# Kernel tuning notes

Hardware: AMD Instinct MI355X
Metric: run time of the kernel (lower is better)

## Reference

```python
import jax, jax.numpy as jnp
import numpy as np

N, E, DIN, DH, H, B = 50000, 800000, 128, 32, 8, 512
NEG_SLOPE = 0.2


def glorot(key, shape):
    fan_in, fan_out = shape[0], shape[-1]
    lim = (6.0 / (fan_in + fan_out)) ** 0.5
    return jax.random.uniform(key, shape, jnp.float32, -lim, lim)


def setup_inputs() -> dict:
    key = jax.random.key(0)
    ks = jax.random.split(key, 16)
    x = jax.random.normal(ks[0], (N, DIN), jnp.float32)
    edge_index = jax.random.randint(ks[1], (2, E), 0, N, jnp.int64)
    batch = jnp.sort(jax.random.randint(ks[2], (N,), 0, B, jnp.int64))
    edge_weight = jax.random.uniform(ks[3], (E, 1), jnp.float32)
    # layer 1: GATv2Conv(DIN -> DH, heads=H, edge_dim=1)
    Wl1 = glorot(ks[4], (DIN, H * DH))
    Wr1 = glorot(ks[5], (DIN, H * DH))
    We1 = glorot(ks[6], (1, H * DH))
    att1 = glorot(ks[7], (H, DH))
    b1 = jnp.zeros((H * DH,), jnp.float32)
    # layer 2: GATv2Conv(H*DH -> DH, heads=1, edge_dim=1)
    Wl2 = glorot(ks[8], (H * DH, DH))
    Wr2 = glorot(ks[9], (H * DH, DH))
    We2 = glorot(ks[10], (1, DH))
    att2 = glorot(ks[11], (1, DH))
    b2 = jnp.zeros((DH,), jnp.float32)
    Wfc = glorot(ks[12], (DH, 1))
    bfc = jnp.zeros((1,), jnp.float32)
    return dict(x=x, edge_index=edge_index, batch=batch, edge_weight=edge_weight,
                Wl1=Wl1, Wr1=Wr1, We1=We1, att1=att1, b1=b1,
                Wl2=Wl2, Wr2=Wr2, We2=We2, att2=att2, b2=b2,
                Wfc=Wfc, bfc=bfc)


def gatv2_layer(x, src, dst, ew, Wl, Wr, We, att, bias, heads, out_ch):
    n = x.shape[0]
    xl = (x @ Wl).reshape(n, heads, out_ch)   # source transform
    xr = (x @ Wr).reshape(n, heads, out_ch)   # target transform
    ee = (ew @ We).reshape(-1, heads, out_ch)  # edge attr transform
    z = xl[src] + xr[dst] + ee                 # [E,H,C]
    s = jnp.einsum('ehc,hc->eh', jax.nn.leaky_relu(z, NEG_SLOPE), att)
    # segment softmax over edges sharing the same target node
    m = jax.ops.segment_max(s, dst, num_segments=n)
    ex = jnp.exp(s - m[dst])
    den = jax.ops.segment_sum(ex, dst, num_segments=n)
    alpha = ex / (den[dst] + 1e-16)            # [E,H]
    out = jax.ops.segment_sum(alpha[..., None] * xl[src], dst, num_segments=n)
    return out.reshape(n, heads * out_ch) + bias


def add_self_loops(edge_index, edge_weight, n):
    loops = jnp.arange(n, dtype=edge_index.dtype)
    src = jnp.concatenate([edge_index[0], loops])
    dst = jnp.concatenate([edge_index[1], loops])
    fill = jnp.mean(edge_weight, axis=0, keepdims=True)  # fill_value='mean'
    ew = jnp.concatenate([edge_weight, jnp.broadcast_to(fill, (n, edge_weight.shape[1]))])
    return src, dst, ew


def reference(x, edge_index, batch, edge_weight,
              Wl1, Wr1, We1, att1, b1,
              Wl2, Wr2, We2, att2, b2,
              Wfc, bfc):
    n = x.shape[0]
    src, dst, ew = add_self_loops(edge_index, edge_weight, n)
    h = gatv2_layer(x, src, dst, ew, Wl1, Wr1, We1, att1, b1, H, DH)
    h = jax.nn.relu(h)
    h = gatv2_layer(h, src, dst, ew, Wl2, Wr2, We2, att2, b2, 1, DH)
    feat = jax.nn.relu(h)
    # global mean pool over graphs
    sums = jax.ops.segment_sum(feat, batch, num_segments=B)
    cnt = jax.ops.segment_sum(jnp.ones((n, 1), feat.dtype), batch, num_segments=B)
    feat = sums / jnp.maximum(cnt, 1.0)
    feat = jax.nn.sigmoid(feat)
    return feat @ Wfc + bfc  # [B,1]
```

## Files before the change

kernel.cpp:

```cpp
#include <hip/hip_runtime.h>
#include <math.h>

#define N_NODES 50000
#define N_EDGES 800000
#define D_IN    128
#define D_H     32
#define N_HEADS 8
#define N_GRAPHS 512
#define E_TOT   (N_EDGES + N_NODES)
#define HDIM    (N_HEADS * D_H)
#define NEG_SLOPE 0.2f
#define NSCAN_BLK ((N_NODES + 255) / 256)
#define LOG2E 1.4426950408889634f
#define RESCALE_THR2 11.0f

typedef short bfrag8 __attribute__((ext_vector_type(8)));
typedef float f32x4 __attribute__((ext_vector_type(4)));
typedef float f32x2 __attribute__((ext_vector_type(2)));

#if __has_builtin(__builtin_amdgcn_exp2f)
#define EXP2(x) __builtin_amdgcn_exp2f(x)
#else
#define EXP2(x) exp2f(x)
#endif

__device__ __forceinline__ unsigned short f2b(float x) {
    unsigned u = __float_as_uint(x);
    unsigned r = u + 0x7FFFu + ((u >> 16) & 1u);
    return (unsigned short)(r >> 16);
}
__device__ __forceinline__ f32x2 b2x2(unsigned u) {
    f32x2 v;
    v.x = __uint_as_float(u << 16);
    v.y = __uint_as_float(u & 0xFFFF0000u);
    return v;
}

__device__ __forceinline__ float dpp8_sum(float x) {
    x += __int_as_float(__builtin_amdgcn_mov_dpp(__float_as_int(x), 0xB1, 0xF, 0xF, true));
    x += __int_as_float(__builtin_amdgcn_mov_dpp(__float_as_int(x), 0x4E, 0xF, 0xF, true));
    x += __int_as_float(__builtin_amdgcn_mov_dpp(__float_as_int(x), 0x141, 0xF, 0xF, true));
    return x;
}

#define RS_BLK   512
#define HIST_BLK ((E_TOT + 255) / 256)
#define W1_BLK   (512 * 128 / 256)
#define W2_BLK   (64 * 256 / 256)
__global__ void k_front(const float* __restrict__ ew, const int* __restrict__ ei,
                        const float* __restrict__ Wl1, const float* __restrict__ Wr1,
                        const float* __restrict__ Wl2, const float* __restrict__ Wr2,
                        float* __restrict__ fillsum, int* __restrict__ deg,
                        unsigned short* __restrict__ Wt1,
                        unsigned short* __restrict__ Wt2) {
    __shared__ float ls[4];
    int b = blockIdx.x;
    if (b < RS_BLK) {
        int t = b * 256 + threadIdx.x;
        float s = 0.f;
        for (int i = t; i < N_EDGES; i += RS_BLK * 256) s += ew[i];
        for (int m = 1; m < 64; m <<= 1) s += __shfl_xor(s, m);
        int lane = threadIdx.x & 63, wv = threadIdx.x >> 6;
        if (lane == 0) ls[wv] = s;
        __syncthreads();
        if (threadIdx.x == 0) atomicAdd(fillsum, ls[0] + ls[1] + ls[2] + ls[3]);
    } else if (b < RS_BLK + HIST_BLK) {
        int e = (b - RS_BLK) * 256 + threadIdx.x;
        if (e >= E_TOT) return;
        int dst = (e < N_EDGES) ? ei[N_EDGES + e] : (e - N_EDGES);
        atomicAdd(&deg[dst], 1);
    } else if (b < RS_BLK + HIST_BLK + W1_BLK) {
        int t = (b - RS_BLK - HIST_BLK) * 256 + threadIdx.x;
        int c = t >> 7, k = t & 127;
        float v = (c < 256) ? Wl1[k * 256 + c] : Wr1[k * 256 + (c - 256)];
        Wt1[t] = f2b(v);
    } else {
        int t = (b - RS_BLK - HIST_BLK - W1_BLK) * 256 + threadIdx.x;
        int c = t >> 8, k = t & 255;
        float v = (c < 32) ? Wl2[k * 32 + c] : Wr2[k * 32 + (c - 32)];
        Wt2[t] = f2b(v);
    }
}

__global__ void k_scan1(const int* __restrict__ deg, int* __restrict__ start,
                        int* __restrict__ bsum) {
    __shared__ int sh[256];
    int i = blockIdx.x * 256 + threadIdx.x;
    int v = (i < N_NODES) ? deg[i] : 0;
    sh[threadIdx.x] = v;
    __syncthreads();
    for (int o = 1; o < 256; o <<= 1) {
        int t = (threadIdx.x >= o) ? sh[threadIdx.x - o] : 0;
        __syncthreads();
        sh[threadIdx.x] += t;
        __syncthreads();
    }
    if (i < N_NODES) start[i] = sh[threadIdx.x] - v;
    if (threadIdx.x == 255) bsum[blockIdx.x] = sh[255];
}
__global__ void k_scan2(int* __restrict__ bsum, int nb) {
    __shared__ int sh[256];
    int v = (threadIdx.x < nb) ? bsum[threadIdx.x] : 0;
    sh[threadIdx.x] = v;
    __syncthreads();
    for (int o = 1; o < 256; o <<= 1) {
        int t = (threadIdx.x >= o) ? sh[threadIdx.x - o] : 0;
        __syncthreads();
        sh[threadIdx.x] += t;
        __syncthreads();
    }
    if (threadIdx.x < nb) bsum[threadIdx.x] = sh[threadIdx.x] - v;
}
__global__ void k_scan3(int* __restrict__ start, const int* __restrict__ bsum,
                        int* __restrict__ cur, int2* __restrict__ csr) {
    int i = blockIdx.x * 256 + threadIdx.x;
    if (i < N_NODES) {
        int v = start[i] + bsum[blockIdx.x];
        start[i] = v;
        cur[i] = v;
    }
    if (i == 0) {
        csr[E_TOT]     = make_int2(0, 0);
        csr[E_TOT + 1] = make_int2(0, 0);
        csr[E_TOT + 2] = make_int2(0, 0);
        csr[E_TOT + 3] = make_int2(0, 0);
    }
}

#define G1_BLOCKS 1564
#define SC_BLOCKS ((E_TOT + 255) / 256)
#define HY_TOT    4985
__global__ __launch_bounds__(256) void k_gemm1_scatter(
    const float* __restrict__ A, const unsigned short* __restrict__ Bt,
    unsigned short* __restrict__ C,
    const int* __restrict__ ei, const float* __restrict__ ew,
    const float* __restrict__ fillsum, int* __restrict__ cur,
    int2* __restrict__ csr)
{
    const int KC = 128, NN = 512, M = N_NODES;
    __shared__ unsigned short A_lds[128][KC + 8];
    __shared__ unsigned short B_lds[128][KC + 8];
    int bid = blockIdx.x;
    int tid = threadIdx.x;
    if (bid % 3 != 0) {
        int sid = bid - bid / 3 - 1;
        if (sid >= SC_BLOCKS) return;
        int e = sid * 256 + tid;
        if (e >= E_TOT) return;
        int src, dst; float w;
        if (e < N_EDGES) { src = ei[e]; dst = ei[N_EDGES + e]; w = ew[e]; }
        else { src = dst = e - N_EDGES; w = fillsum[0] * (1.0f / N_EDGES); }
        int pos = atomicAdd(&cur[dst], 1);
        csr[pos] = make_int2(src, __float_as_int(w));
        return;
    }
    int gid = bid / 3;
    if (gid >= G1_BLOCKS) return;
    int row0 = (gid >> 2) * 128, col0 = (gid & 3) * 128;
    for (int idx = tid; idx < 128 * 32; idx += 256) {
        int r = idx >> 5, c4 = idx & 31;
        int gr = row0 + r;
        float4 v = {0.f, 0.f, 0.f, 0.f};
        if (gr < M) v = ((const float4*)(A + (size_t)gr * KC))[c4];
        ushort4 o;
        o.x = f2b(v.x); o.y = f2b(v.y); o.z = f2b(v.z); o.w = f2b(v.w);
        *(ushort4*)&A_lds[r][c4 * 4] = o;
    }
    for (int idx = tid; idx < 128 * 16; idx += 256) {
        int r = idx >> 4, ch = idx & 15;
        uint4 v = *(const uint4*)(Bt + (size_t)(col0 + r) * KC + ch * 8);
        *(uint4*)&B_lds[r][ch * 8] = v;
    }
    __syncthreads();

    int wid = tid >> 6, lane = tid & 63;
    int wy = wid >> 1, wx = wid & 1;
    int lr = lane & 15, lh = lane >> 4;
    f32x4 acc[4][4] = {};
    #pragma unroll
    for (int k0 = 0; k0 < KC; k0 += 32) {
        bfrag8 af[4], bf[4];
        #pragma unroll
        for (int i = 0; i < 4; ++i) {
            af[i] = *(const bfrag8*)&A_lds[64 * wy + 16 * i + lr][k0 + lh * 8];
            bf[i] = *(const bfrag8*)&B_lds[64 * wx + 16 * i + lr][k0 + lh * 8];
        }
        #pragma unroll
        for (int mi = 0; mi < 4; ++mi)
            #pragma unroll
            for (int ni = 0; ni < 4; ++ni)
                acc[mi][ni] = __builtin_amdgcn_mfma_f32_16x16x32_bf16(af[mi], bf[ni], acc[mi][ni], 0, 0, 0);
    }
    #pragma unroll
    for (int mi = 0; mi < 4; ++mi) {
        #pragma unroll
        for (int ni = 0; ni < 4; ++ni) {
            #pragma unroll
            for (int r = 0; r < 4; ++r) {
                int row = row0 + 64 * wy + 16 * mi + lh * 4 + r;
                if (row < M)
                    C[(size_t)row * NN + col0 + 64 * wx + 16 * ni + lr] = f2b(acc[mi][ni][r]);
            }
        }
    }
}

__global__ __launch_bounds__(256) void k_gemm2(
    const unsigned short* __restrict__ A, const unsigned short* __restrict__ Bt,
    unsigned short* __restrict__ C, int M)
{
    const int KC = 256, NN = 64;
    __shared__ unsigned short A_lds[64][KC + 8];
    __shared__ unsigned short B_lds[64][KC + 8];
    int row0 = blockIdx.y * 64, col0 = 0;
    int tid = threadIdx.x;
    const int CPR = KC / 8;
    for (int idx = tid; idx < 64 * CPR; idx += 256) {
        int r = idx / CPR, ch = idx % CPR;
        int gr = row0 + r;
        uint4 v = {0u, 0u, 0u, 0u};
        if (gr < M) v = *(const uint4*)(A + (size_t)gr * KC + ch * 8);
        *(uint4*)&A_lds[r][ch * 8] = v;
    }
    for (int idx = tid; idx < 64 * CPR; idx += 256) {
        int r = idx / CPR, ch = idx % CPR;
        uint4 v = *(const uint4*)(Bt + (size_t)(col0 + r) * KC + ch * 8);
        *(uint4*)&B_lds[r][ch * 8] = v;
    }
    __syncthreads();

    int wid = tid >> 6, lane = tid & 63;
    int wy = wid >> 1, wx = wid & 1;
    int lr = lane & 15, lh = lane >> 4;
    f32x4 acc[2][2] = {};
    #pragma unroll
    for (int k0 = 0; k0 < KC; k0 += 32) {
        bfrag8 a0 = *(const bfrag8*)&A_lds[32 * wy + lr][k0 + lh * 8];
        bfrag8 a1 = *(const bfrag8*)&A_lds[32 * wy + 16 + lr][k0 + lh * 8];
        bfrag8 b0 = *(const bfrag8*)&B_lds[32 * wx + lr][k0 + lh * 8];
        bfrag8 b1 = *(const bfrag8*)&B_lds[32 * wx + 16 + lr][k0 + lh * 8];
        acc[0][0] = __builtin_amdgcn_mfma_f32_16x16x32_bf16(a0, b0, acc[0][0], 0, 0, 0);
        acc[0][1] = __builtin_amdgcn_mfma_f32_16x16x32_bf16(a0, b1, acc[0][1], 0, 0, 0);
        acc[1][0] = __builtin_amdgcn_mfma_f32_16x16x32_bf16(a1, b0, acc[1][0], 0, 0, 0);
        acc[1][1] = __builtin_amdgcn_mfma_f32_16x16x32_bf16(a1, b1, acc[1][1], 0, 0, 0);
    }
    #pragma unroll
    for (int mt = 0; mt < 2; ++mt) {
        #pragma unroll
        for (int nt = 0; nt < 2; ++nt) {
            #pragma unroll
            for (int r = 0; r < 4; ++r) {
                int row = row0 + 32 * wy + 16 * mt + lh * 4 + r;
                if (row < M)
                    C[(size_t)row * NN + col0 + 32 * wx + 16 * nt + lr] = f2b(acc[mt][nt][r]);
            }
        }
    }
}

__global__ __launch_bounds__(256) void k_gat1(
    const unsigned short* __restrict__ xlr,
    const int* __restrict__ start, const int* __restrict__ deg,
    const int2* __restrict__ csr,
    const float* __restrict__ We, const float* __restrict__ att,
    const float* __restrict__ b1, unsigned short* __restrict__ out1)
{
    int wid = (blockIdx.x * blockDim.x + threadIdx.x) >> 6;
    int lane = threadIdx.x & 63;
    if (wid >= N_NODES) return;
    f32x2 we01 = ((const f32x2*)We)[2 * lane],  we23 = ((const f32x2*)We)[2 * lane + 1];
    f32x2 at01 = ((const f32x2*)att)[2 * lane], at23 = ((const f32x2*)att)[2 * lane + 1];
    at01 *= LOG2E; at23 *= LOG2E;
    uint2 xru = *(const uint2*)(xlr + (size_t)wid * 512 + 256 + 4 * lane);
    f32x2 xr01 = b2x2(xru.x), xr23 = b2x2(xru.y);
    int s0 = start[wid], dg = deg[wid];
    const int2* ep = csr + s0;
    float m = -1e30f, d = 0.f;
    f32x2 acc01 = {0.f, 0.f}, acc23 = {0.f, 0.f};

    int2 e0 = ep[0], e1 = ep[1], e2 = ep[2], e3 = ep[3];
    uint2 r0 = *(const uint2*)(xlr + ((size_t)e0.x << 9) + 4 * lane);
    uint2 r1 = *(const uint2*)(xlr + ((size_t)e1.x << 9) + 4 * lane);
    uint2 r2 = *(const uint2*)(xlr + ((size_t)e2.x << 9) + 4 * lane);
    uint2 r3 = *(const uint2*)(xlr + ((size_t)e3.x << 9) + 4 * lane);

    for (int j = 0; j < dg; j += 4) {
        float w0 = __int_as_float(e0.y), w1 = __int_as_float(e1.y);
        float w2 = __int_as_float(e2.y), w3 = __int_as_float(e3.y);
        f32x2 a001 = b2x2(r0.x), a023 = b2x2(r0.y);
        f32x2 a101 = b2x2(r1.x), a123 = b2x2(r1.y);
        f32x2 a201 = b2x2(r2.x), a223 = b2x2(r2.y);
        f32x2 a301 = b2x2(r3.x), a323 = b2x2(r3.y);
        int jn = j + 4;
        if (jn < dg) {
            e0 = ep[jn]; e1 = ep[jn + 1]; e2 = ep[jn + 2]; e3 = ep[jn + 3];
            r0 = *(const uint2*)(xlr + ((size_t)e0.x << 9) + 4 * lane);
            r1 = *(const uint2*)(xlr + ((size_t)e1.x << 9) + 4 * lane);
            r2 = *(const uint2*)(xlr + ((size_t)e2.x << 9) + 4 * lane);
            r3 = *(const uint2*)(xlr + ((size_t)e3.x << 9) + 4 * lane);
        }
        f32x2 z, lz, ww, pv;
        ww = (f32x2){w0, w0}; pv = (f32x2){0.f, 0.f};
        z = a001 + __builtin_elementwise_fma(ww, we01, xr01);
        lz = __builtin_elementwise_max(z, z * NEG_SLOPE);
        pv = __builtin_elementwise_fma(lz, at01, pv);
        z = a023 + __builtin_elementwise_fma(ww, we23, xr23);
        lz = __builtin_elementwise_max(z, z * NEG_SLOPE);
        pv = __builtin_elementwise_fma(lz, at23, pv);
        float p0 = pv.x + pv.y;
        ww = (f32x2){w1, w1}; pv = (f32x2){0.f, 0.f};
        z = a101 + __builtin_elementwise_fma(ww, we01, xr01);
        lz = __builtin_elementwise_max(z, z * NEG_SLOPE);
        pv = __builtin_elementwise_fma(lz, at01, pv);
        z = a123 + __builtin_elementwise_fma(ww, we23, xr23);
        lz = __builtin_elementwise_max(z, z * NEG_SLOPE);
        pv = __builtin_elementwise_fma(lz, at23, pv);
        float p1 = pv.x + pv.y;
        ww = (f32x2){w2, w2}; pv = (f32x2){0.f, 0.f};
        z = a201 + __builtin_elementwise_fma(ww, we01, xr01);
        lz = __builtin_elementwise_max(z, z * NEG_SLOPE);
        pv = __builtin_elementwise_fma(lz, at01, pv);
        z = a223 + __builtin_elementwise_fma(ww, we23, xr23);
        lz = __builtin_elementwise_max(z, z * NEG_SLOPE);
        pv = __builtin_elementwise_fma(lz, at23, pv);
        float p2 = pv.x + pv.y;
        ww = (f32x2){w3, w3}; pv = (f32x2){0.f, 0.f};
        z = a301 + __builtin_elementwise_fma(ww, we01, xr01);
        lz = __builtin_elementwise_max(z, z * NEG_SLOPE);
        pv = __builtin_elementwise_fma(lz, at01, pv);
        z = a323 + __builtin_elementwise_fma(ww, we23, xr23);
        lz = __builtin_elementwise_max(z, z * NEG_SLOPE);
        pv = __builtin_elementwise_fma(lz, at23, pv);
        float p3 = pv.x + pv.y;
        p0 = dpp8_sum(p0); p1 = dpp8_sum(p1);
        p2 = dpp8_sum(p2); p3 = dpp8_sum(p3);
        if (j + 1 >= dg) p1 = -1e30f;
        if (j + 2 >= dg) p2 = -1e30f;
        if (j + 3 >= dg) p3 = -1e30f;
        float pm = fmaxf(fmaxf(p0, p1), fmaxf(p2, p3));
        if (__any(pm > m + RESCALE_THR2)) {
            float nm = fmaxf(m, pm);
            float sc = EXP2(m - nm);
            d *= sc;
            acc01 *= sc; acc23 *= sc;
            m = nm;
        }
        float q0 = EXP2(p0 - m), q1 = EXP2(p1 - m);
        float q2 = EXP2(p2 - m), q3 = EXP2(p3 - m);
        d += (q0 + q1) + (q2 + q3);
        f32x2 qq;
        qq = (f32x2){q0, q0};
        acc01 = __builtin_elementwise_fma(qq, a001, acc01);
        acc23 = __builtin_elementwise_fma(qq, a023, acc23);
        qq = (f32x2){q1, q1};
        acc01 = __builtin_elementwise_fma(qq, a101, acc01);
        acc23 = __builtin_elementwise_fma(qq, a123, acc23);
        qq = (f32x2){q2, q2};
        acc01 = __builtin_elementwise_fma(qq, a201, acc01);
        acc23 = __builtin_elementwise_fma(qq, a223, acc23);
        qq = (f32x2){q3, q3};
        acc01 = __builtin_elementwise_fma(qq, a301, acc01);
        acc23 = __builtin_elementwise_fma(qq, a323, acc23);
    }
    float inv = 1.f / (d + 1e-16f);
    f32x2 b01 = ((const f32x2*)b1)[2 * lane], b23 = ((const f32x2*)b1)[2 * lane + 1];
    ushort4 o;
    o.x = f2b(fmaxf(fmaf(acc01.x, inv, b01.x), 0.f));
    o.y = f2b(fmaxf(fmaf(acc01.y, inv, b01.y), 0.f));
    o.z = f2b(fmaxf(fmaf(acc23.x, inv, b23.x), 0.f));
    o.w = f2b(fmaxf(fmaf(acc23.y, inv, b23.y), 0.f));
    *(ushort4*)(out1 + (size_t)wid * 256 + 4 * lane) = o;
}

__global__ __launch_bounds__(256) void k_gat2(
    const unsigned short* __restrict__ xlr2,
    const int* __restrict__ start, const int* __restrict__ deg,
    const int2* __restrict__ csr,
    const float* __restrict__ We, const float* __restrict__ att,
    const float* __restrict__ b2, const int* __restrict__ batch,
    float* __restrict__ pool, float* __restrict__ cnt)
{
    int gt = blockIdx.x * blockDim.x + threadIdx.x;
    int i = gt >> 3, g = gt & 7;
    if (i >= N_NODES) return;
    f32x2 we01 = ((const f32x2*)We)[2 * g],  we23 = ((const f32x2*)We)[2 * g + 1];
    f32x2 at01 = ((const f32x2*)att)[2 * g], at23 = ((const f32x2*)att)[2 * g + 1];
    at01 *= LOG2E; at23 *= LOG2E;
    uint2 xru = *(const uint2*)(xlr2 + (size_t)i * 64 + 32 + 4 * g);
    f32x2 xr01 = b2x2(xru.x), xr23 = b2x2(xru.y);
    int s0 = start[i], dg = deg[i];
    const int2* ep = csr + s0;
    float m = -1e30f, d = 0.f;
    f32x2 acc01 = {0.f, 0.f}, acc23 = {0.f, 0.f};

    int2 ec0 = ep[0], ec1 = ep[1];
    uint2 ra0 = *(const uint2*)(xlr2 + ((size_t)ec0.x << 6) + 4 * g);
    uint2 ra1 = *(const uint2*)(xlr2 + ((size_t)ec1.x << 6) + 4 * g);

    for (int j = 0; j < dg; j += 2) {
        int2 c0 = ec0, c1 = ec1;
        uint2 A0 = ra0, A1 = ra1;
        int jn = j + 2;
        if (jn < dg) {
            ec0 = ep[jn]; ec1 = ep[jn + 1];
            ra0 = *(const uint2*)(xlr2 + ((size_t)ec0.x << 6) + 4 * g);
            ra1 = *(const uint2*)(xlr2 + ((size_t)ec1.x << 6) + 4 * g);
        }
        float w0 = __int_as_float(c0.y), w1 = __int_as_float(c1.y);
        f32x2 ww0 = {w0, w0}, ww1 = {w1, w1};
        f32x2 a001 = b2x2(A0.x), a023 = b2x2(A0.y);
        f32x2 a101 = b2x2(A1.x), a123 = b2x2(A1.y);
        f32x2 p0v = {0.f, 0.f}, p1v = {0.f, 0.f}, z, lz;
        z = a001 + __builtin_elementwise_fma(ww0, we01, xr01);
        lz = __builtin_elementwise_max(z, z * NEG_SLOPE);
        p0v = __builtin_elementwise_fma(lz, at01, p0v);
        z = a023 + __builtin_elementwise_fma(ww0, we23, xr23);
        lz = __builtin_elementwise_max(z, z * NEG_SLOPE);
        p0v = __builtin_elementwise_fma(lz, at23, p0v);
        z = a101 + __builtin_elementwise_fma(ww1, we01, xr01);
        lz = __builtin_elementwise_max(z, z * NEG_SLOPE);
        p1v = __builtin_elementwise_fma(lz, at01, p1v);
        z = a123 + __builtin_elementwise_fma(ww1, we23, xr23);
        lz = __builtin_elementwise_max(z, z * NEG_SLOPE);
        p1v = __builtin_elementwise_fma(lz, at23, p1v);
        float p0 = dpp8_sum(p0v.x + p0v.y);
        float p1 = dpp8_sum(p1v.x + p1v.y);
        if (j + 1 >= dg) p1 = -1e30f;
        float pm = fmaxf(p0, p1);
        if (__any(pm > m + RESCALE_THR2)) {
            float nm = fmaxf(m, pm);
            float sc = EXP2(m - nm);
            d *= sc;
            acc01 *= sc; acc23 *= sc;
            m = nm;
        }
        float q0 = EXP2(p0 - m), q1 = EXP2(p1 - m);
        d += q0 + q1;
        f32x2 qq0 = {q0, q0}, qq1 = {q1, q1};
        acc01 = __builtin_elementwise_fma(qq0, a001, acc01);
        acc23 = __builtin_elementwise_fma(qq0, a023, acc23);
        acc01 = __builtin_elementwise_fma(qq1, a101, acc01);
        acc23 = __builtin_elementwise_fma(qq1, a123, acc23);
    }
    float inv = 1.f / (d + 1e-16f);
    f32x2 b01 = ((const f32x2*)b2)[2 * g], b23 = ((const f32x2*)b2)[2 * g + 1];
    float vx = fmaxf(fmaf(acc01.x, inv, b01.x), 0.f);
    float vy = fmaxf(fmaf(acc01.y, inv, b01.y), 0.f);
    float vz = fmaxf(fmaf(acc23.x, inv, b23.x), 0.f);
    float vw = fmaxf(fmaf(acc23.y, inv, b23.y), 0.f);
    int b = batch[i];
    float* o = pool + (size_t)b * D_H + g * 4;
    atomicAdd(o + 0, vx);
    atomicAdd(o + 1, vy);
    atomicAdd(o + 2, vz);
    atomicAdd(o + 3, vw);
    if (g == 0) atomicAdd(&cnt[b], 1.0f);
}

__global__ void k_final(const float* __restrict__ pool, const float* __restrict__ cnt,
                        const float* __restrict__ Wfc, const float* __restrict__ bfc,
                        float* __restrict__ out)
{
    int b = blockIdx.x * blockDim.x + threadIdx.x;
    if (b >= N_GRAPHS) return;
    float c = cnt[b]; c = c > 1.f ? c : 1.f;
    float acc = 0.f;
    #pragma unroll
    for (int j = 0; j < D_H; ++j) {
        float f = pool[b * D_H + j] / c;
        f = 1.f / (1.f + __expf(-f));
        acc = fmaf(f, Wfc[j], acc);
    }
    out[b] = acc + bfc[0];
}

extern "C" void kernel_launch(void* const* d_in, const int* in_sizes, int n_in,
                              void* d_out, int out_size, void* d_ws, size_t ws_size,
                              hipStream_t stream)
{
    const float* x    = (const float*)d_in[0];
    const int*   ei   = (const int*)  d_in[1];
    const int*   batch= (const int*)  d_in[2];
    const float* ew   = (const float*)d_in[3];
    const float* Wl1  = (const float*)d_in[4];
    const float* Wr1  = (const float*)d_in[5];
    const float* We1  = (const float*)d_in[6];
    const float* att1 = (const float*)d_in[7];
    const float* b1   = (const float*)d_in[8];
    const float* Wl2  = (const float*)d_in[9];
    const float* Wr2  = (const float*)d_in[10];
    const float* We2  = (const float*)d_in[11];
    const float* att2 = (const float*)d_in[12];
    const float* b2   = (const float*)d_in[13];
    const float* Wfc  = (const float*)d_in[14];
    const float* bfc  = (const float*)d_in[15];
    float* out = (float*)d_out;

    float* ws = (float*)d_ws;
    size_t off = 0;
    auto take = [&](size_t n) -> float* {
        float* p = ws + off;
        off = (off + n + 63) & ~(size_t)63;
        return p;
    };
    float* fillsum = take(1);
    int*   deg  = (int*)take(N_NODES);
    float* cnt  = take(N_GRAPHS);
    float* pool = take((size_t)N_GRAPHS * D_H);
    size_t zero_elems = off;
    int*   start = (int*)take(N_NODES);
    int*   cur   = (int*)take(N_NODES);
    int*   bsum  = (int*)take(256);
    int2*  csr   = (int2*)take((size_t)(E_TOT + 4) * 2);
    unsigned short* Wt1  = (unsigned short*)take(512 * 128 / 2);
    unsigned short* Wt2  = (unsigned short*)take(64 * 256 / 2);
    unsigned short* xlr1 = (unsigned short*)take((size_t)N_NODES * 512 / 2);
    unsigned short* out1 = (unsigned short*)take((size_t)N_NODES * 256 / 2);
    unsigned short* xlr2 = (unsigned short*)take((size_t)N_NODES * 64 / 2);
    (void)ws_size; (void)in_sizes; (void)n_in; (void)out_size;

    hipMemsetAsync(d_ws, 0, zero_elems * sizeof(float), stream);

    k_front<<<RS_BLK + HIST_BLK + W1_BLK + W2_BLK, 256, 0, stream>>>(
        ew, ei, Wl1, Wr1, Wl2, Wr2, fillsum, deg, Wt1, Wt2);

    k_scan1<<<NSCAN_BLK, 256, 0, stream>>>(deg, start, bsum);
    k_scan2<<<1, 256, 0, stream>>>(bsum, NSCAN_BLK);
    k_scan3<<<NSCAN_BLK, 256, 0, stream>>>(start, bsum, cur, csr);

    k_gemm1_scatter<<<HY_TOT, 256, 0, stream>>>(
        x, Wt1, xlr1, ei, ew, fillsum, cur, csr);

    k_gat1<<<(N_NODES * 64 + 255) / 256, 256, 0, stream>>>(
        xlr1, start, deg, csr, We1, att1, b1, out1);

    k_gemm2<<<dim3(1, (N_NODES + 63) / 64), 256, 0, stream>>>(
        out1, Wt2, xlr2, N_NODES);

    k_gat2<<<((size_t)N_NODES * 8 + 255) / 256, 256, 0, stream>>>(
        xlr2, start, deg, csr, We2, att2, b2, batch, pool, cnt);

    k_final<<<(N_GRAPHS + 255) / 256, 256, 0, stream>>>(pool, cnt, Wfc, bfc, out);
}
```

Measured before the change: 277.4 us.

## Record histogram ranks for atomic-free CSR scatter and split gat2 edges across two lanes

The degree histogram now stores each edge's atomic return value as a rank, so the CSR scatter computes its position as start[dst] + rank[e] and needs no second atomic pass or cursor array. Layer-2 attention now uses 16 lanes per node instead of 8. Two half-groups process interleaved edge pairs and merge their online-softmax state with a cross-lane shuffle before the pooling atomics. This adds an E_TOT rank buffer, extra masking for tail edges, and more csr padding for the wider prefetch.

```diff
diff --git a/kernel.cpp b/kernel.cpp
--- a/kernel.cpp
+++ b/kernel.cpp
@@ -51,6 +51,7 @@
                         const float* __restrict__ Wl1, const float* __restrict__ Wr1,
                         const float* __restrict__ Wl2, const float* __restrict__ Wr2,
                         float* __restrict__ fillsum, int* __restrict__ deg,
+                        int* __restrict__ rank,
                         unsigned short* __restrict__ Wt1,
                         unsigned short* __restrict__ Wt2) {
     __shared__ float ls[4];
@@ -68,7 +69,7 @@
         int e = (b - RS_BLK) * 256 + threadIdx.x;
         if (e >= E_TOT) return;
         int dst = (e < N_EDGES) ? ei[N_EDGES + e] : (e - N_EDGES);
-        atomicAdd(&deg[dst], 1);
+        rank[e] = atomicAdd(&deg[dst], 1);
     } else if (b < RS_BLK + HIST_BLK + W1_BLK) {
         int t = (b - RS_BLK - HIST_BLK) * 256 + threadIdx.x;
         int c = t >> 7, k = t & 127;
@@ -112,18 +113,12 @@
     if (threadIdx.x < nb) bsum[threadIdx.x] = sh[threadIdx.x] - v;
 }
 __global__ void k_scan3(int* __restrict__ start, const int* __restrict__ bsum,
-                        int* __restrict__ cur, int2* __restrict__ csr) {
+                        int2* __restrict__ csr) {
     int i = blockIdx.x * 256 + threadIdx.x;
-    if (i < N_NODES) {
-        int v = start[i] + bsum[blockIdx.x];
-        start[i] = v;
-        cur[i] = v;
-    }
+    if (i < N_NODES) start[i] += bsum[blockIdx.x];
     if (i == 0) {
-        csr[E_TOT]     = make_int2(0, 0);
-        csr[E_TOT + 1] = make_int2(0, 0);
-        csr[E_TOT + 2] = make_int2(0, 0);
-        csr[E_TOT + 3] = make_int2(0, 0);
+        #pragma unroll
+        for (int k = 0; k < 8; ++k) csr[E_TOT + k] = make_int2(0, 0);
     }
 }
 
@@ -134,8 +129,8 @@
     const float* __restrict__ A, const unsigned short* __restrict__ Bt,
     unsigned short* __restrict__ C,
     const int* __restrict__ ei, const float* __restrict__ ew,
-    const float* __restrict__ fillsum, int* __restrict__ cur,
-    int2* __restrict__ csr)
+    const float* __restrict__ fillsum, const int* __restrict__ start,
+    const int* __restrict__ rank, int2* __restrict__ csr)
 {
     const int KC = 128, NN = 512, M = N_NODES;
     __shared__ unsigned short A_lds[128][KC + 8];
@@ -150,7 +145,7 @@
         int src, dst; float w;
         if (e < N_EDGES) { src = ei[e]; dst = ei[N_EDGES + e]; w = ew[e]; }
         else { src = dst = e - N_EDGES; w = fillsum[0] * (1.0f / N_EDGES); }
-        int pos = atomicAdd(&cur[dst], 1);
+        int pos = start[dst] + rank[e];
         csr[pos] = make_int2(src, __float_as_int(w));
         return;
     }
@@ -381,7 +376,10 @@
     float* __restrict__ pool, float* __restrict__ cnt)
 {
     int gt = blockIdx.x * blockDim.x + threadIdx.x;
-    int i = gt >> 3, g = gt & 7;
+    int i = gt >> 4;
+    int sub = gt & 15;
+    int s = sub >> 3;
+    int g = sub & 7;
     if (i >= N_NODES) return;
     f32x2 we01 = ((const f32x2*)We)[2 * g],  we23 = ((const f32x2*)We)[2 * g + 1];
     f32x2 at01 = ((const f32x2*)att)[2 * g], at23 = ((const f32x2*)att)[2 * g + 1];
@@ -393,15 +391,17 @@
     float m = -1e30f, d = 0.f;
     f32x2 acc01 = {0.f, 0.f}, acc23 = {0.f, 0.f};
 
-    int2 ec0 = ep[0], ec1 = ep[1];
+    int T = (dg + 3) >> 2;
+    int2 ec0 = ep[2 * s], ec1 = ep[2 * s + 1];
     uint2 ra0 = *(const uint2*)(xlr2 + ((size_t)ec0.x << 6) + 4 * g);
     uint2 ra1 = *(const uint2*)(xlr2 + ((size_t)ec1.x << 6) + 4 * g);
 
-    for (int j = 0; j < dg; j += 2) {
+    for (int t = 0; t < T; ++t) {
+        int j0 = 4 * t + 2 * s;
         int2 c0 = ec0, c1 = ec1;
         uint2 A0 = ra0, A1 = ra1;
-        int jn = j + 2;
-        if (jn < dg) {
+        if (t + 1 < T) {
+            int jn = 4 * (t + 1) + 2 * s;
             ec0 = ep[jn]; ec1 = ep[jn + 1];
             ra0 = *(const uint2*)(xlr2 + ((size_t)ec0.x << 6) + 4 * g);
             ra1 = *(const uint2*)(xlr2 + ((size_t)ec1.x << 6) + 4 * g);
@@ -425,7 +425,9 @@
         p1v = __builtin_elementwise_fma(lz, at23, p1v);
         float p0 = dpp8_sum(p0v.x + p0v.y);
         float p1 = dpp8_sum(p1v.x + p1v.y);
-        if (j + 1 >= dg) p1 = -1e30f;
+        bool v0 = j0 < dg, v1 = j0 + 1 < dg;
+        if (!v0) p0 = -1e30f;
+        if (!v1) p1 = -1e30f;
         float pm = fmaxf(p0, p1);
         if (__any(pm > m + RESCALE_THR2)) {
             float nm = fmaxf(m, pm);
@@ -434,7 +436,8 @@
             acc01 *= sc; acc23 *= sc;
             m = nm;
         }
-        float q0 = EXP2(p0 - m), q1 = EXP2(p1 - m);
+        float q0 = v0 ? EXP2(p0 - m) : 0.f;
+        float q1 = v1 ? EXP2(p1 - m) : 0.f;
         d += q0 + q1;
         f32x2 qq0 = {q0, q0}, qq1 = {q1, q1};
         acc01 = __builtin_elementwise_fma(qq0, a001, acc01);
@@ -442,19 +445,36 @@
         acc01 = __builtin_elementwise_fma(qq1, a101, acc01);
         acc23 = __builtin_elementwise_fma(qq1, a123, acc23);
     }
-    float inv = 1.f / (d + 1e-16f);
-    f32x2 b01 = ((const f32x2*)b2)[2 * g], b23 = ((const f32x2*)b2)[2 * g + 1];
-    float vx = fmaxf(fmaf(acc01.x, inv, b01.x), 0.f);
-    float vy = fmaxf(fmaf(acc01.y, inv, b01.y), 0.f);
-    float vz = fmaxf(fmaf(acc23.x, inv, b23.x), 0.f);
-    float vw = fmaxf(fmaf(acc23.y, inv, b23.y), 0.f);
-    int b = batch[i];
-    float* o = pool + (size_t)b * D_H + g * 4;
-    atomicAdd(o + 0, vx);
-    atomicAdd(o + 1, vy);
-    atomicAdd(o + 2, vz);
-    atomicAdd(o + 3, vw);
-    if (g == 0) atomicAdd(&cnt[b], 1.0f);
+
+    {
+        float mo = __shfl_xor(m, 8);
+        float dd = __shfl_xor(d, 8);
+        f32x2 ao01, ao23;
+        ao01.x = __shfl_xor(acc01.x, 8); ao01.y = __shfl_xor(acc01.y, 8);
+        ao23.x = __shfl_xor(acc23.x, 8); ao23.y = __shfl_xor(acc23.y, 8);
+        float nm = fmaxf(m, mo);
+        float sa = EXP2(m - nm), sb = EXP2(mo - nm);
+        d = d * sa + dd * sb;
+        f32x2 va = {sa, sa}, vb = {sb, sb};
+        acc01 = acc01 * va + ao01 * vb;
+        acc23 = acc23 * va + ao23 * vb;
+    }
+
+    if (s == 0) {
+        float inv = 1.f / (d + 1e-16f);
+        f32x2 b01 = ((const f32x2*)b2)[2 * g], b23 = ((const f32x2*)b2)[2 * g + 1];
+        float vx = fmaxf(fmaf(acc01.x, inv, b01.x), 0.f);
+        float vy = fmaxf(fmaf(acc01.y, inv, b01.y), 0.f);
+        float vz = fmaxf(fmaf(acc23.x, inv, b23.x), 0.f);
+        float vw = fmaxf(fmaf(acc23.y, inv, b23.y), 0.f);
+        int b = batch[i];
+        float* o = pool + (size_t)b * D_H + g * 4;
+        atomicAdd(o + 0, vx);
+        atomicAdd(o + 1, vy);
+        atomicAdd(o + 2, vz);
+        atomicAdd(o + 3, vw);
+        if (g == 0) atomicAdd(&cnt[b], 1.0f);
+    }
 }
 
 __global__ void k_final(const float* __restrict__ pool, const float* __restrict__ cnt,
@@ -509,9 +529,9 @@
     float* pool = take((size_t)N_GRAPHS * D_H);
     size_t zero_elems = off;
     int*   start = (int*)take(N_NODES);
-    int*   cur   = (int*)take(N_NODES);
+    int*   rank  = (int*)take(E_TOT);
     int*   bsum  = (int*)take(256);
-    int2*  csr   = (int2*)take((size_t)(E_TOT + 4) * 2);
+    int2*  csr   = (int2*)take((size_t)(E_TOT + 8) * 2);
     unsigned short* Wt1  = (unsigned short*)take(512 * 128 / 2);
     unsigned short* Wt2  = (unsigned short*)take(64 * 256 / 2);
     unsigned short* xlr1 = (unsigned short*)take((size_t)N_NODES * 512 / 2);
@@ -522,14 +542,14 @@
     hipMemsetAsync(d_ws, 0, zero_elems * sizeof(float), stream);
 
     k_front<<<RS_BLK + HIST_BLK + W1_BLK + W2_BLK, 256, 0, stream>>>(
-        ew, ei, Wl1, Wr1, Wl2, Wr2, fillsum, deg, Wt1, Wt2);
+        ew, ei, Wl1, Wr1, Wl2, Wr2, fillsum, deg, rank, Wt1, Wt2);
 
     k_scan1<<<NSCAN_BLK, 256, 0, stream>>>(deg, start, bsum);
     k_scan2<<<1, 256, 0, stream>>>(bsum, NSCAN_BLK);
-    k_scan3<<<NSCAN_BLK, 256, 0, stream>>>(start, bsum, cur, csr);
+    k_scan3<<<NSCAN_BLK, 256, 0, stream>>>(start, bsum, csr);
 
     k_gemm1_scatter<<<HY_TOT, 256, 0, stream>>>(
-        x, Wt1, xlr1, ei, ew, fillsum, cur, csr);
+        x, Wt1, xlr1, ei, ew, fillsum, start, rank, csr);
 
     k_gat1<<<(N_NODES * 64 + 255) / 256, 256, 0, stream>>>(
         xlr1, start, deg, csr, We1, att1, b1, out1);
@@ -537,7 +557,7 @@
     k_gemm2<<<dim3(1, (N_NODES + 63) / 64), 256, 0, stream>>>(
         out1, Wt2, xlr2, N_NODES);
 
-    k_gat2<<<((size_t)N_NODES * 8 + 255) / 256, 256, 0, stream>>>(
+    k_gat2<<<((size_t)N_NODES * 16 + 255) / 256, 256, 0, stream>>>(
         xlr2, start, deg, csr, We2, att2, b2, batch, pool, cnt);
 
     k_final<<<(N_GRAPHS + 255) / 256, 256, 0, stream>>>(pool, cnt, Wfc, bfc, out);
```

Measured after the change: 282.1 us. Within noise of the previous version (+1.7%).
